# Optimization experiments

Measured on AMD Instinct MI355X. Metric: run time of the kernel, lower is better.

## Reference

```python
import jax, jax.numpy as jnp
import numpy as np
import math

L, D, H, V, B, S, MR = 8, 768, 12, 32000, 2, 1024, 4
HD = D // H

def setup_inputs() -> dict:
    key = jax.random.key(0)
    ks = iter(jax.random.split(key, 64))
    def rn(shape, s=0.02):
        return jax.random.normal(next(ks), shape, jnp.float32) * s
    inp = {}
    inp['tokens'] = jax.random.randint(next(ks), (B, S), 0, V, jnp.int32)
    inp['tok_emb'] = rn((V, D))
    inp['pos_emb'] = rn((S, D))
    for n in ['Wq_row', 'Wk_row', 'Wv_row', 'Wq_col', 'Wo']:
        inp[n] = rn((L, D, D))
    for n in ['bq_row', 'bk_row', 'bv_row', 'bq_col', 'bo']:
        inp[n] = jnp.zeros((L, D), jnp.float32)
    inp['ln1_g'] = jnp.ones((L, D), jnp.float32); inp['ln1_b'] = jnp.zeros((L, D), jnp.float32)
    inp['ln2_g'] = jnp.ones((L, D), jnp.float32); inp['ln2_b'] = jnp.zeros((L, D), jnp.float32)
    inp['W1'] = rn((L, D, MR * D)); inp['b1'] = jnp.zeros((L, MR * D), jnp.float32)
    inp['W2'] = rn((L, MR * D, D)); inp['b2'] = jnp.zeros((L, D), jnp.float32)
    inp['Wk_sh'] = rn((D, D)); inp['bk_sh'] = jnp.zeros((D,), jnp.float32)
    inp['Wv_sh'] = rn((D, D)); inp['bv_sh'] = jnp.zeros((D,), jnp.float32)
    inp['lnf_g'] = jnp.ones((D,), jnp.float32); inp['lnf_b'] = jnp.zeros((D,), jnp.float32)
    inp['Whead'] = rn((D, V)); inp['bhead'] = jnp.zeros((V,), jnp.float32)
    return inp

def _ln(x, g, b, eps=1e-5):
    m = x.mean(-1, keepdims=True)
    v = ((x - m) ** 2).mean(-1, keepdims=True)
    return (x - m) * jax.lax.rsqrt(v + eps) * g + b

def _heads(x):
    b, s, _ = x.shape
    return x.reshape(b, s, H, HD).transpose(0, 2, 1, 3)  # [B,H,S,hd]

def _merge(x):
    b, h, s, hd = x.shape
    return x.transpose(0, 2, 1, 3).reshape(b, s, h * hd)

def _forward(tokens, tok_emb, pos_emb, Wq_row, bq_row, Wk_row, bk_row, Wv_row, bv_row,
             Wq_col, bq_col, Wo, bo, ln1_g, ln1_b, ln2_g, ln2_b, W1, b1, W2, b2,
             Wk_sh, bk_sh, Wv_sh, bv_sh, lnf_g, lnf_b, Whead, bhead):
    s_len = tokens.shape[1]
    inv = 1.0 / math.sqrt(HD)
    x = tok_emb[tokens] + pos_emb[:s_len]
    mask = jnp.triu(jnp.ones((s_len, s_len), bool), 1)
    past_k, past_v = [], []
    for i in range(L):
        h = _ln(x, ln1_g[i], ln1_b[i])
        q_row = _heads(h @ Wq_row[i] + bq_row[i])
        k_row = _heads(h @ Wk_row[i] + bk_row[i])
        v_row = _heads(h @ Wv_row[i] + bv_row[i])
        q_col = _heads(h @ Wq_col[i] + bq_col[i])
        k_col = _heads(h @ Wk_sh + bk_sh)   # shared KV projector (archived memory)
        v_col = _heads(h @ Wv_sh + bv_sh)
        ts = jnp.einsum('bhqd,bhkd->bhqk', q_row, k_row) * inv
        ts = jnp.where(mask, -jnp.inf, ts)
        if past_k:
            pk = jnp.stack(past_k, axis=3)  # [B,H,S,l,hd]
            pv = jnp.stack(past_v, axis=3)
            ms = jnp.einsum('bhsd,bhsld->bhsl', q_col, pk) * inv
            w = jax.nn.softmax(jnp.concatenate([ts, ms], axis=-1), axis=-1)
            tw, mw = w[..., :s_len], w[..., s_len:]
            ctx = (jnp.einsum('bhqk,bhkd->bhqd', tw, v_row)
                   + jnp.einsum('bhsl,bhsld->bhsd', mw, pv))
        else:
            ctx = jnp.einsum('bhqk,bhkd->bhqd', jax.nn.softmax(ts, axis=-1), v_row)
        x = x + (_merge(ctx) @ Wo[i] + bo[i])
        h2 = _ln(x, ln2_g[i], ln2_b[i])
        x = x + (jax.nn.gelu(h2 @ W1[i] + b1[i], approximate=False) @ W2[i] + b2[i])
        past_k.append(k_col)
        past_v.append(v_col)
    return _ln(x, lnf_g, lnf_b) @ Whead + bhead

def reference(tokens, tok_emb, pos_emb, Wq_row, bq_row, Wk_row, bk_row, Wv_row, bv_row,
              Wq_col, bq_col, Wo, bo, ln1_g, ln1_b, ln2_g, ln2_b, W1, b1, W2, b2,
              Wk_sh, bk_sh, Wv_sh, bv_sh, lnf_g, lnf_b, Whead, bhead):
    return _forward(tokens, tok_emb, pos_emb, Wq_row, bq_row, Wk_row, bk_row, Wv_row, bv_row,
                    Wq_col, bq_col, Wo, bo, ln1_g, ln1_b, ln2_g, ln2_b, W1, b1, W2, b2,
                    Wk_sh, bk_sh, Wv_sh, bv_sh, lnf_g, lnf_b, Whead, bhead)
```

## Files before the change

### kernel.cpp

```cpp
#include <hip/hip_runtime.h>
#include <hip/hip_bf16.h>
#include <math.h>

#define L_   8
#define D_   768
#define H_   12
#define V_   32000
#define B_   2
#define S_   1024
#define HD_  64
#define BS_  2048
#define DFF_ 3072

typedef __hip_bfloat16 bf16;
typedef __attribute__((ext_vector_type(8))) short bf16x8;
typedef __attribute__((ext_vector_type(4))) float f32x4;

#define CFUN(r) (((r) >> 1) & 3)

__device__ __forceinline__ void cp16(void* lds, const void* g) {
  __builtin_amdgcn_global_load_lds(
      (const __attribute__((address_space(1))) void*)g,
      (__attribute__((address_space(3))) void*)lds, 16, 0, 0);
}

__device__ __forceinline__ unsigned short f2bf(float v) {
  __hip_bfloat16 h = __float2bfloat16(v);
  return *reinterpret_cast<unsigned short*>(&h);
}
__device__ __forceinline__ float bf2f(unsigned short u) {
  return __uint_as_float(((unsigned)u) << 16);
}

__global__ __launch_bounds__(256) void k_embed(const int* __restrict__ tokens,
    const float* __restrict__ tok_emb, const float* __restrict__ pos_emb,
    float* __restrict__ x) {
  int idx = blockIdx.x * 256 + threadIdx.x;
  int row = idx / D_;
  int d   = idx - row * D_;
  int s   = row & (S_ - 1);
  int t   = tokens[row];
  x[idx] = tok_emb[(size_t)t * D_ + d] + pos_emb[(size_t)s * D_ + d];
}

__global__ __launch_bounds__(256) void k_ln(const float* __restrict__ x,
    const float* __restrict__ g, const float* __restrict__ b,
    bf16* __restrict__ out) {
  int row = blockIdx.x;
  const float* xr = x + (size_t)row * D_;
  int t = threadIdx.x;
  float v0 = xr[t], v1 = xr[t + 256], v2 = xr[t + 512];
  float s  = v0 + v1 + v2;
  float s2 = v0 * v0 + v1 * v1 + v2 * v2;
#pragma unroll
  for (int off = 32; off; off >>= 1) {
    s  += __shfl_down(s, off);
    s2 += __shfl_down(s2, off);
  }
  __shared__ float rs[4], rs2[4];
  __shared__ float mean_s, rstd_s;
  int wid = t >> 6;
  if ((t & 63) == 0) { rs[wid] = s; rs2[wid] = s2; }
  __syncthreads();
  if (t == 0) {
    float S1 = rs[0] + rs[1] + rs[2] + rs[3];
    float S2 = rs2[0] + rs2[1] + rs2[2] + rs2[3];
    float m  = S1 / D_;
    float var = S2 / D_ - m * m;
    mean_s = m;
    rstd_s = rsqrtf(var + 1e-5f);
  }
  __syncthreads();
  float m = mean_s, r = rstd_s;
  bf16* orow = out + (size_t)row * D_;
  orow[t]       = __float2bfloat16((v0 - m) * r * g[t]       + b[t]);
  orow[t + 256] = __float2bfloat16((v1 - m) * r * g[t + 256] + b[t + 256]);
  orow[t + 512] = __float2bfloat16((v2 - m) * r * g[t + 512] + b[t + 512]);
}

__global__ __launch_bounds__(256) void k_redln(float* __restrict__ x,
    const float* __restrict__ pk, const float* __restrict__ b2,
    const float* __restrict__ g, const float* __restrict__ b,
    bf16* __restrict__ out) {
  const int row = blockIdx.x;
  const int t = threadIdx.x;
  const size_t base = (size_t)row * D_;
  const size_t MN = (size_t)BS_ * D_;
  float v0, v1, v2;
  {
    int c0 = t, c1 = t + 256, c2 = t + 512;
    v0 = x[base + c0] + pk[base + c0] + pk[MN + base + c0] + b2[c0];
    v1 = x[base + c1] + pk[base + c1] + pk[MN + base + c1] + b2[c1];
    v2 = x[base + c2] + pk[base + c2] + pk[MN + base + c2] + b2[c2];
    x[base + c0] = v0; x[base + c1] = v1; x[base + c2] = v2;
  }
  float s  = v0 + v1 + v2;
  float s2 = v0 * v0 + v1 * v1 + v2 * v2;
#pragma unroll
  for (int off = 32; off; off >>= 1) {
    s  += __shfl_down(s, off);
    s2 += __shfl_down(s2, off);
  }
  __shared__ float rs[4], rs2[4];
  __shared__ float mean_s, rstd_s;
  int wid = t >> 6;
  if ((t & 63) == 0) { rs[wid] = s; rs2[wid] = s2; }
  __syncthreads();
  if (t == 0) {
    float S1 = rs[0] + rs[1] + rs[2] + rs[3];
    float S2 = rs2[0] + rs2[1] + rs2[2] + rs2[3];
    float m  = S1 / D_;
    float var = S2 / D_ - m * m;
    mean_s = m;
    rstd_s = rsqrtf(var + 1e-5f);
  }
  __syncthreads();
  float m = mean_s, r = rstd_s;
  bf16* orow = out + base;
  orow[t]       = __float2bfloat16((v0 - m) * r * g[t]       + b[t]);
  orow[t + 256] = __float2bfloat16((v1 - m) * r * g[t + 256] + b[t + 256]);
  orow[t + 512] = __float2bfloat16((v2 - m) * r * g[t + 512] + b[t + 512]);
}

__global__ __launch_bounds__(256) void k_w2bf_t(const float* __restrict__ W,
    bf16* __restrict__ Wt, int K, int N, size_t ils, size_t ols) {
  __shared__ float t[32][33];
  const float* Wm = W + (size_t)blockIdx.z * ils;
  bf16* Wtm = Wt + (size_t)blockIdx.z * ols;
  int n0 = blockIdx.x * 32, k0 = blockIdx.y * 32;
  int tx = threadIdx.x;
  for (int i = threadIdx.y; i < 32; i += 8)
    t[i][tx] = Wm[(size_t)(k0 + i) * N + n0 + tx];
  __syncthreads();
  for (int i = threadIdx.y; i < 32; i += 8)
    Wtm[(size_t)(n0 + i) * K + k0 + tx] = __float2bfloat16(t[tx][i]);
}

__global__ __launch_bounds__(256) void k_bcat(const float* __restrict__ bq,
    const float* __restrict__ bk, const float* __restrict__ bqc,
    const float* __restrict__ bv, const float* __restrict__ bksh,
    const float* __restrict__ bvsh, float* __restrict__ b6) {
  int idx = blockIdx.x * 256 + threadIdx.x;
  if (idx >= L_ * 4608) return;
  int l = idx / 4608, c = idx - l * 4608;
  float v = (c < 768)  ? bq[l * 768 + c]
          : (c < 1536) ? bk[l * 768 + c - 768]
          : (c < 2304) ? bqc[l * 768 + c - 1536]
          : (c < 3072) ? bv[l * 768 + c - 2304]
          : (c < 3840) ? bksh[c - 3072]
                       : bvsh[c - 3840];
  b6[idx] = v;
}

template <int BM, int EPI, int KSPL>
__global__ __launch_bounds__(256) void k_bgemm(
    const bf16* __restrict__ A, const bf16* __restrict__ Wt,
    const bf16* __restrict__ Wt2,
    const float* __restrict__ bias, const float* __restrict__ resid,
    float* __restrict__ Cf, bf16* __restrict__ Cb, bf16* __restrict__ Cb2,
    bf16* __restrict__ Cb3, int NM, int M, int N, int K) {
  constexpr int ASZ = BM * 64;
  constexpr int ALINES = BM / 64;
  constexpr int BSTRIDE = ASZ + 8192;
  constexpr int MF = BM / 32;
  __shared__ __align__(16) char smem[3 * BSTRIDE];
  const int tid = threadIdx.x;
  const int l = tid & 63, w = tid >> 6;
  const int wr = w >> 1, wc = w & 1;

  const int nwg = (int)gridDim.x;
  int id = (int)blockIdx.x;
  id = (id & 7) * (nwg >> 3) + (id >> 3);
  int sk = 0;
  if constexpr (KSPL == 2) {
    const int TT = nwg >> 1;
    sk = id / TT;
    id -= sk * TT;
  }
  const int m0 = (id % NM) * BM;
  const int n0 = (id / NM) * 128;
  const int kstart = sk * (K / KSPL);

  const int lane15 = l & 15, lg = l >> 4;

  const bf16* WB = Wt;
  int nb0 = n0;
  if constexpr (EPI == 6) {
    if (n0 >= 3072) { WB = Wt2; nb0 = n0 - 3072; }
  }

  const int r0 = tid >> 2, p0 = tid & 3;
  const char* aSrc[ALINES];
#pragma unroll
  for (int i = 0; i < ALINES; i++) {
    const int rr = i * 64 + r0;
    aSrc[i] = (const char*)(A + (size_t)(m0 + rr) * K + kstart) + ((p0 ^ CFUN(rr)) * 16);
  }
  const char* bSrc0 = (const char*)(WB + (size_t)(nb0 + r0) * K + kstart) + ((p0 ^ CFUN(r0)) * 16);
  const char* bSrc1 = (const char*)(WB + (size_t)(nb0 + 64 + r0) * K + kstart) + ((p0 ^ CFUN(64 + r0)) * 16);

  int aOff[MF], bOff[4];
#pragma unroll
  for (int mi = 0; mi < MF; mi++) {
    int r = wr * (BM / 2) + mi * 16 + lane15;
    aOff[mi] = r * 64 + ((lg ^ CFUN(r)) * 16);
  }
#pragma unroll
  for (int ni = 0; ni < 4; ni++) {
    int r = wc * 64 + ni * 16 + lane15;
    bOff[ni] = ASZ + r * 64 + ((lg ^ CFUN(r)) * 16);
  }

  f32x4 acc[MF][4];
#pragma unroll
  for (int mi = 0; mi < MF; mi++)
#pragma unroll
    for (int ni = 0; ni < 4; ni++) acc[mi][ni] = (f32x4){0.f, 0.f, 0.f, 0.f};

  auto stage = [&](int buf, int t) {
    const size_t kb = (size_t)t * 64;
    char* base = smem + buf * BSTRIDE;
#pragma unroll
    for (int i = 0; i < ALINES; i++)
      cp16(base + i * 4096 + w * 1024, aSrc[i] + kb);
    cp16(base + ASZ + w * 1024, bSrc0 + kb);
    cp16(base + ASZ + 4096 + w * 1024, bSrc1 + kb);
  };
  auto compute = [&](int buf) {
    const char* base = smem + buf * BSTRIDE;
    bf16x8 af[MF], bfr[4];
#pragma unroll
    for (int mi = 0; mi < MF; mi++) af[mi] = *(const bf16x8*)(base + aOff[mi]);
#pragma unroll
    for (int ni = 0; ni < 4; ni++) bfr[ni] = *(const bf16x8*)(base + bOff[ni]);
    __builtin_amdgcn_s_setprio(1);
#pragma unroll
    for (int mi = 0; mi < MF; mi++)
#pragma unroll
      for (int ni = 0; ni < 4; ni++)
        acc[mi][ni] = __builtin_amdgcn_mfma_f32_16x16x32_bf16(
            af[mi], bfr[ni], acc[mi][ni], 0, 0, 0);
    __builtin_amdgcn_s_setprio(0);
  };

  const int nk = (K / KSPL) >> 5;
  stage(0, 0);
  stage(1, 1);
  int buf = 0;
  for (int t = 0; t < nk; t++) {
    if (t + 1 < nk) {
      if constexpr (ALINES == 2) asm volatile("s_waitcnt vmcnt(4)" ::: "memory");
      else                       asm volatile("s_waitcnt vmcnt(3)" ::: "memory");
    } else {
      asm volatile("s_waitcnt vmcnt(0)" ::: "memory");
    }
    __builtin_amdgcn_s_barrier();
    if (t + 2 < nk) {
      int nb = buf + 2; if (nb >= 3) nb -= 3;
      stage(nb, t + 2);
    }
    compute(buf);
    buf = (buf == 2) ? 0 : buf + 1;
  }

#pragma unroll
  for (int ni = 0; ni < 4; ni++) {
    const int col = n0 + wc * 64 + ni * 16 + lane15;
    const float bv = bias[col];
#pragma unroll
    for (int mi = 0; mi < MF; mi++) {
      const int rowb = m0 + wr * (BM / 2) + mi * 16 + lg * 4;
      if constexpr (EPI == 6) {
        if (col < 2304) {
#pragma unroll
          for (int j = 0; j < 4; j++)
            Cb[(size_t)(rowb + j) * 2304 + col] = __float2bfloat16(acc[mi][ni][j] + bv);
        } else if (col < 3072) {
          ushort4 pk;
          pk.x = f2bf(acc[mi][ni][0] + bv);
          pk.y = f2bf(acc[mi][ni][1] + bv);
          pk.z = f2bf(acc[mi][ni][2] + bv);
          pk.w = f2bf(acc[mi][ni][3] + bv);
          const int bq = rowb >> 10, s = rowb & (S_ - 1);
          *reinterpret_cast<ushort4*>(
              (unsigned short*)Cb2 + ((size_t)(bq * 768 + (col - 2304))) * S_ + s) = pk;
        } else {
#pragma unroll
          for (int j = 0; j < 4; j++)
            Cb3[(size_t)(rowb + j) * 1536 + (col - 3072)] =
                __float2bfloat16(acc[mi][ni][j] + bv);
        }
      } else if constexpr (EPI == 7) {
#pragma unroll
        for (int j = 0; j < 4; j++)
          Cf[(size_t)sk * M * N + (size_t)(rowb + j) * N + col] = acc[mi][ni][j];
      } else {
#pragma unroll
        for (int j = 0; j < 4; j++) {
          const int row = rowb + j;
          float v = acc[mi][ni][j] + bv;
          if constexpr (EPI == 1) v += resid[(size_t)row * N + col];
          if constexpr (EPI == 2) {
            v = 0.5f * v * (1.0f + erff(v * 0.70710678118654752f));
            Cb[(size_t)row * N + col] = __float2bfloat16(v);
          } else if constexpr (EPI == 3) {
            Cb[(size_t)row * N + col] = __float2bfloat16(v);
          } else {
            Cf[(size_t)row * N + col] = v;
          }
        }
      }
    }
  }
}

#define HBAR() asm volatile("s_barrier" ::: "memory")
#define MFMA16(AF, BF, MB, NB)                                               \
  do {                                                                       \
    __builtin_amdgcn_s_setprio(1);                                           \
    _Pragma("unroll") for (int mi_ = 0; mi_ < 4; mi_++)                      \
      _Pragma("unroll") for (int ni_ = 0; ni_ < 2; ni_++)                    \
        _Pragma("unroll") for (int ks_ = 0; ks_ < 2; ks_++)                  \
          acc[(MB) + mi_][(NB) + ni_] =                                      \
              __builtin_amdgcn_mfma_f32_16x16x32_bf16(                       \
                  AF[mi_][ks_], BF[ni_][ks_], acc[(MB) + mi_][(NB) + ni_],   \
                  0, 0, 0);                                                  \
    __builtin_amdgcn_s_setprio(0);                                           \
  } while (0)

__global__ __launch_bounds__(512, 1) void k_head8(const bf16* __restrict__ A,
    const bf16* __restrict__ Wt, const float* __restrict__ bias,
    float* __restrict__ C) {
  __shared__ __align__(16) char smem[131072];
  const int tid = threadIdx.x;
  const int l = tid & 63, w = tid >> 6;
  const int wr = w >> 2, wc = w & 3;
  const int lane15 = l & 15, lg = l >> 4;

  int id = (int)blockIdx.x;
  id = (id & 7) * 125 + (id >> 3);
  const int m0 = (id % 8) * 256;
  const int n0 = (id / 8) * 256;

  auto issueA = [&](int tile, int hb) {
#pragma unroll
    for (int j = 0; j < 2; j++) {
      const int idx = j * 512 + tid;
      const int rl = idx >> 3, sl = idx & 7;
      const bf16* g = A + (size_t)(m0 + hb + rl) * 768 + tile * 64 +
                      ((sl ^ (rl & 7)) << 3);
      cp16(smem + (tile & 1) * 32768 + hb * 128 + (j * 512 + w * 64) * 16, g);
    }
  };
  auto issueB = [&](int tile, int hb) {
#pragma unroll
    for (int j = 0; j < 2; j++) {
      const int idx = j * 512 + tid;
      const int rl = idx >> 3, sl = idx & 7;
      const bf16* g = Wt + (size_t)(n0 + hb + rl) * 768 + tile * 64 +
                      ((sl ^ (rl & 7)) << 3);
      cp16(smem + 65536 + (tile & 1) * 32768 + hb * 128 + (j * 512 + w * 64) * 16, g);
    }
  };
  auto ldA = [&](int buf, int mi, int ks) {
    const int r = wr * 128 + mi * 16 + lane15;
    return *(const bf16x8*)(smem + buf * 32768 + r * 128 +
                            ((((ks << 2) + lg) ^ (r & 7)) << 4));
  };
  auto ldB = [&](int buf, int ni, int ks) {
    const int r = wc * 64 + ni * 16 + lane15;
    return *(const bf16x8*)(smem + 65536 + buf * 32768 + r * 128 +
                            ((((ks << 2) + lg) ^ (r & 7)) << 4));
  };

  f32x4 acc[8][4];
#pragma unroll
  for (int i = 0; i < 8; i++)
#pragma unroll
    for (int j = 0; j < 4; j++) acc[i][j] = (f32x4){0.f, 0.f, 0.f, 0.f};
  bf16x8 alo[4][2], ahi[4][2], blo[2][2], bhi[2][2];

  issueA(0, 0);  issueA(0, 128);  issueB(0, 0);  issueB(0, 128);
  issueB(1, 0);  issueA(1, 0);    issueB(1, 128);
  asm volatile("s_waitcnt vmcnt(6)" ::: "memory");
  HBAR();

  for (int it = 0; it < 5; ++it) {
    const int Tb = 2 * it + 1, Tn = 2 * it + 2;
#pragma unroll
    for (int mi = 0; mi < 4; mi++) { alo[mi][0] = ldA(0, mi, 0); alo[mi][1] = ldA(0, mi, 1); }
#pragma unroll
    for (int ni = 0; ni < 2; ni++) { blo[ni][0] = ldB(0, ni, 0); blo[ni][1] = ldB(0, ni, 1); }
    issueA(Tb, 128);
    HBAR(); MFMA16(alo, blo, 0, 0); HBAR();
#pragma unroll
    for (int ni = 0; ni < 2; ni++) { bhi[ni][0] = ldB(0, ni + 2, 0); bhi[ni][1] = ldB(0, ni + 2, 1); }
    HBAR(); MFMA16(alo, bhi, 0, 2); HBAR();
#pragma unroll
    for (int mi = 0; mi < 4; mi++) { ahi[mi][0] = ldA(0, mi + 4, 0); ahi[mi][1] = ldA(0, mi + 4, 1); }
    issueB(Tn, 0);
    HBAR(); MFMA16(ahi, bhi, 4, 2); HBAR();
    issueA(Tn, 0);
    issueB(Tn, 128);
    asm volatile("s_waitcnt vmcnt(6)" ::: "memory");
    HBAR(); MFMA16(ahi, blo, 4, 0); HBAR();
#pragma unroll
    for (int mi = 0; mi < 4; mi++) { alo[mi][0] = ldA(1, mi, 0); alo[mi][1] = ldA(1, mi, 1); }
#pragma unroll
    for (int ni = 0; ni < 2; ni++) { blo[ni][0] = ldB(1, ni, 0); blo[ni][1] = ldB(1, ni, 1); }
    issueA(Tn, 128);
    HBAR(); MFMA16(alo, blo, 0, 0); HBAR();
#pragma unroll
    for (int ni = 0; ni < 2; ni++) { bhi[ni][0] = ldB(1, ni + 2, 0); bhi[ni][1] = ldB(1, ni + 2, 1); }
    HBAR(); MFMA16(alo, bhi, 0, 2); HBAR();
#pragma unroll
    for (int mi = 0; mi < 4; mi++) { ahi[mi][0] = ldA(1, mi + 4, 0); ahi[mi][1] = ldA(1, mi + 4, 1); }
    issueB(Tn + 1, 0);
    HBAR(); MFMA16(ahi, bhi, 4, 2); HBAR();
    issueA(Tn + 1, 0);
    issueB(Tn + 1, 128);
    asm volatile("s_waitcnt vmcnt(6)" ::: "memory");
    HBAR(); MFMA16(ahi, blo, 4, 0); HBAR();
  }

  {
#pragma unroll
    for (int mi = 0; mi < 4; mi++) { alo[mi][0] = ldA(0, mi, 0); alo[mi][1] = ldA(0, mi, 1); }
#pragma unroll
    for (int ni = 0; ni < 2; ni++) { blo[ni][0] = ldB(0, ni, 0); blo[ni][1] = ldB(0, ni, 1); }
    issueA(11, 128);
    HBAR(); MFMA16(alo, blo, 0, 0); HBAR();
#pragma unroll
    for (int ni = 0; ni < 2; ni++) { bhi[ni][0] = ldB(0, ni + 2, 0); bhi[ni][1] = ldB(0, ni + 2, 1); }
    HBAR(); MFMA16(alo, bhi, 0, 2); HBAR();
#pragma unroll
    for (int mi = 0; mi < 4; mi++) { ahi[mi][0] = ldA(0, mi + 4, 0); ahi[mi][1] = ldA(0, mi + 4, 1); }
    HBAR(); MFMA16(ahi, bhi, 4, 2); HBAR();
    asm volatile("s_waitcnt vmcnt(0)" ::: "memory");
    HBAR(); MFMA16(ahi, blo, 4, 0); HBAR();
#pragma unroll
    for (int mi = 0; mi < 4; mi++) { alo[mi][0] = ldA(1, mi, 0); alo[mi][1] = ldA(1, mi, 1); }
#pragma unroll
    for (int ni = 0; ni < 2; ni++) { blo[ni][0] = ldB(1, ni, 0); blo[ni][1] = ldB(1, ni, 1); }
    MFMA16(alo, blo, 0, 0);
#pragma unroll
    for (int ni = 0; ni < 2; ni++) { bhi[ni][0] = ldB(1, ni + 2, 0); bhi[ni][1] = ldB(1, ni + 2, 1); }
    MFMA16(alo, bhi, 0, 2);
#pragma unroll
    for (int mi = 0; mi < 4; mi++) { ahi[mi][0] = ldA(1, mi + 4, 0); ahi[mi][1] = ldA(1, mi + 4, 1); }
    MFMA16(ahi, bhi, 4, 2);
    MFMA16(ahi, blo, 4, 0);
  }

#pragma unroll
  for (int ni = 0; ni < 4; ni++) {
    const int col = n0 + wc * 64 + ni * 16 + lane15;
    const float bv = bias[col];
#pragma unroll
    for (int mi = 0; mi < 8; mi++) {
      const int rowb = m0 + wr * 128 + mi * 16 + lg * 4;
#pragma unroll
      for (int j = 0; j < 4; j++)
        C[(size_t)(rowb + j) * 32000 + col] = acc[mi][ni][j] + bv;
    }
  }
}

__global__ __launch_bounds__(256) void k_attn(
    const bf16* __restrict__ qkv, const bf16* __restrict__ vT,
    const bf16* __restrict__ memkv, bf16* __restrict__ ctx, int layer) {
  const int bh = blockIdx.x;
  const int b = bh / H_, h = bh % H_;
  const int qt = (int)gridDim.y - 1 - (int)blockIdx.y;
  const int tid = threadIdx.x;
  const int w = tid >> 6, l = tid & 63;
  const int lane15 = l & 15, lg = l >> 4;
  const float inv = 0.125f;

  __shared__ char plds[4][2048];
  __shared__ float wlp[4][16][16];
  char* pl = plds[w];

  const int qrow0 = qt * 64 + w * 16;
  const size_t rowA = (size_t)(b * S_ + qrow0 + lane15);
  const bf16* qp = qkv + rowA * 2304 + h * 64 + lg * 8;
  auto scale8 = [](bf16x8 v) {
    bf16x8 r;
#pragma unroll
    for (int e = 0; e < 8; e++)
      r[e] = (short)f2bf(bf2f((unsigned short)v[e]) * 0.125f);
    return r;
  };
  const bf16x8 qf0 = scale8(*(const bf16x8*)(qp));
  const bf16x8 qf1 = scale8(*(const bf16x8*)(qp + 32));

  const bf16* kbase = qkv + (size_t)(b * S_) * 2304 + 768 + h * 64 + lg * 8;
  const bf16* vbase = vT + ((size_t)(b * 768 + h * 64 + lane15)) * S_;

  float mrow[4], dsum[4];
  f32x4 acc[4];
#pragma unroll
  for (int j = 0; j < 4; j++) { mrow[j] = -INFINITY; dsum[j] = 0.f; }
#pragma unroll
  for (int ni = 0; ni < 4; ni++) acc[ni] = (f32x4){0.f, 0.f, 0.f, 0.f};

  const int ntile = ((qrow0 + 15) >> 6) + 1;
  for (int kt64 = 0; kt64 < ntile; kt64++) {
    const int k0 = kt64 * 64;
    f32x4 sc[4];
#pragma unroll
    for (int kt = 0; kt < 4; kt++) {
      const bf16* kp = kbase + (size_t)(k0 + kt * 16 + lane15) * 2304;
      bf16x8 kf0 = *(const bf16x8*)(kp);
      bf16x8 kf1 = *(const bf16x8*)(kp + 32);
      f32x4 z = (f32x4){0.f, 0.f, 0.f, 0.f};
      z = __builtin_amdgcn_mfma_f32_16x16x32_bf16(qf0, kf0, z, 0, 0, 0);
      sc[kt] = __builtin_amdgcn_mfma_f32_16x16x32_bf16(qf1, kf1, z, 0, 0, 0);
    }
    float tmax[4];
#pragma unroll
    for (int j = 0; j < 4; j++) tmax[j] = -INFINITY;
    const bool needMask = (k0 + 63 > qrow0);
    if (needMask) {
#pragma unroll
      for (int kt = 0; kt < 4; kt++) {
        const int kabs = k0 + kt * 16 + lane15;
#pragma unroll
        for (int j = 0; j < 4; j++) {
          const int qabs = qrow0 + lg * 4 + j;
          float v = (kabs <= qabs) ? sc[kt][j] : -INFINITY;
          sc[kt][j] = v;
          tmax[j] = fmaxf(tmax[j], v);
        }
      }
    } else {
#pragma unroll
      for (int kt = 0; kt < 4; kt++)
#pragma unroll
        for (int j = 0; j < 4; j++) tmax[j] = fmaxf(tmax[j], sc[kt][j]);
    }
#pragma unroll
    for (int off = 1; off < 16; off <<= 1)
#pragma unroll
      for (int j = 0; j < 4; j++) tmax[j] = fmaxf(tmax[j], __shfl_xor(tmax[j], off, 16));

    bool grow = false;
#pragma unroll
    for (int j = 0; j < 4; j++) grow |= (tmax[j] > mrow[j]);
    if (__ballot(grow) != 0ull) {
#pragma unroll
      for (int j = 0; j < 4; j++) {
        const float mnew = fmaxf(mrow[j], tmax[j]);
        const float alpha = __expf(mrow[j] - mnew);
        mrow[j] = mnew;
        dsum[j] *= alpha;
#pragma unroll
        for (int ni = 0; ni < 4; ni++) acc[ni][j] *= alpha;
      }
    }
    float psum[4] = {0.f, 0.f, 0.f, 0.f};
#pragma unroll
    for (int kt = 0; kt < 4; kt++) {
      const int gsl = kt * 2 + (lane15 >> 3);
      const int ebyte = (lane15 & 7) * 2;
#pragma unroll
      for (int j = 0; j < 4; j++) {
        const float p = __expf(sc[kt][j] - mrow[j]);
        psum[j] += p;
        const int r = lg * 4 + j;
        *(unsigned short*)(pl + r * 128 + ((gsl ^ (r & 7)) << 4) + ebyte) = f2bf(p);
      }
    }
#pragma unroll
    for (int off = 1; off < 16; off <<= 1)
#pragma unroll
      for (int j = 0; j < 4; j++) psum[j] += __shfl_xor(psum[j], off, 16);
#pragma unroll
    for (int j = 0; j < 4; j++) dsum[j] += psum[j];

#pragma unroll
    for (int ks = 0; ks < 2; ks++) {
      bf16x8 pa = *(const bf16x8*)(pl + lane15 * 128 +
                                   ((((ks << 2) + lg) ^ (lane15 & 7)) << 4));
      const bf16* vp = vbase + k0 + ks * 32 + lg * 8;
#pragma unroll
      for (int ni = 0; ni < 4; ni++) {
        bf16x8 vf = *(const bf16x8*)(vp + (size_t)ni * 16 * S_);
        acc[ni] = __builtin_amdgcn_mfma_f32_16x16x32_bf16(pa, vf, acc[ni], 0, 0, 0);
      }
    }
  }

  const int r4 = lg * 4;
  if (lane15 < layer) {
    const int ml = lane15;
#pragma unroll
    for (int j = 0; j < 4; j++) {
      const size_t rowB = (size_t)(b * S_) + qrow0 + r4 + j;
      const bf16* qc = qkv + rowB * 2304 + 1536 + h * 64;
      const bf16* mk = memkv + ((size_t)ml * BS_ + rowB) * 1536 + h * 64;
      float d_ = 0.f;
#pragma unroll
      for (int t = 0; t < 8; t++) {
        bf16x8 qv = *(const bf16x8*)(qc + t * 8);
        bf16x8 kv = *(const bf16x8*)(mk + t * 8);
#pragma unroll
        for (int e = 0; e < 8; e++)
          d_ += bf2f((unsigned short)qv[e]) * bf2f((unsigned short)kv[e]);
      }
      wlp[w][r4 + j][ml] = d_ * inv;
    }
  }
  if (layer > 0) {
#pragma unroll
    for (int j = 0; j < 4; j++) {
      const int r = r4 + j;
      float mm = -INFINITY;
      for (int ml = 0; ml < layer; ml++) mm = fmaxf(mm, wlp[w][r][ml]);
      const float mnew = fmaxf(mrow[j], mm);
      const float alpha = __expf(mrow[j] - mnew);
      mrow[j] = mnew;
      dsum[j] *= alpha;
#pragma unroll
      for (int ni = 0; ni < 4; ni++) acc[ni][j] *= alpha;
      const size_t rowB = (size_t)(b * S_) + qrow0 + r;
      for (int ml = 0; ml < layer; ml++) {
        const float p = __expf(wlp[w][r][ml] - mnew);
        dsum[j] += p;
        const unsigned short* mv = (const unsigned short*)(memkv +
            ((size_t)ml * BS_ + rowB) * 1536 + 768 + h * 64 + lane15);
#pragma unroll
        for (int ni = 0; ni < 4; ni++)
          acc[ni][j] += p * bf2f(mv[ni * 16]);
      }
    }
  }

#pragma unroll
  for (int j = 0; j < 4; j++) {
    const float rd = 1.f / dsum[j];
    const size_t rowB = (size_t)(b * S_) + qrow0 + r4 + j;
    bf16* cp = ctx + rowB * 768 + h * 64 + lane15;
#pragma unroll
    for (int ni = 0; ni < 4; ni++)
      cp[ni * 16] = __float2bfloat16(acc[ni][j] * rd);
  }
}

extern "C" void kernel_launch(void* const* d_in, const int* in_sizes, int n_in,
                              void* d_out, int out_size, void* d_ws, size_t ws_size,
                              hipStream_t stream) {
  const int*   tokens  = (const int*)d_in[0];
  const float* tok_emb = (const float*)d_in[1];
  const float* pos_emb = (const float*)d_in[2];
  const float *Wq_row, *Wk_row, *Wv_row, *Wq_col, *Wo;
  const float *bq_row, *bk_row, *bv_row, *bq_col, *bo;
  if (in_sizes[4] == L_ * D_ * D_) {
    Wq_row = (const float*)d_in[3];  Wk_row = (const float*)d_in[4];
    Wv_row = (const float*)d_in[5];  Wq_col = (const float*)d_in[6];
    Wo     = (const float*)d_in[7];
    bq_row = (const float*)d_in[8];  bk_row = (const float*)d_in[9];
    bv_row = (const float*)d_in[10]; bq_col = (const float*)d_in[11];
    bo     = (const float*)d_in[12];
  } else {
    Wq_row = (const float*)d_in[3];  bq_row = (const float*)d_in[4];
    Wk_row = (const float*)d_in[5];  bk_row = (const float*)d_in[6];
    Wv_row = (const float*)d_in[7];  bv_row = (const float*)d_in[8];
    Wq_col = (const float*)d_in[9];  bq_col = (const float*)d_in[10];
    Wo     = (const float*)d_in[11]; bo     = (const float*)d_in[12];
  }
  const float* ln1_g = (const float*)d_in[13]; const float* ln1_b = (const float*)d_in[14];
  const float* ln2_g = (const float*)d_in[15]; const float* ln2_b = (const float*)d_in[16];
  const float* W1    = (const float*)d_in[17]; const float* b1    = (const float*)d_in[18];
  const float* W2    = (const float*)d_in[19]; const float* b2    = (const float*)d_in[20];
  const float* Wk_sh = (const float*)d_in[21]; const float* bk_sh = (const float*)d_in[22];
  const float* Wv_sh = (const float*)d_in[23]; const float* bv_sh = (const float*)d_in[24];
  const float* lnf_g = (const float*)d_in[25]; const float* lnf_b = (const float*)d_in[26];
  const float* Whead = (const float*)d_in[27]; const float* bhead = (const float*)d_in[28];

  char* p = (char*)d_ws;
  float* x      = (float*)p; p += (size_t)BS_ * D_ * 4;
  bf16*  h_bf   = (bf16*)p;  p += (size_t)BS_ * D_ * 2;
  bf16*  qkv3   = (bf16*)p;  p += (size_t)BS_ * 2304 * 2;
  bf16*  vTb    = (bf16*)p;  p += (size_t)B_ * 768 * S_ * 2;
  bf16*  memkv  = (bf16*)p;  p += (size_t)L_ * BS_ * 1536 * 2;
  bf16*  ctx_bf = (bf16*)p;  p += (size_t)BS_ * D_ * 2;
  bf16*  mlp_bf = (bf16*)p;  p += (size_t)BS_ * DFF_ * 2;
  float* pkbuf  = (float*)p; p += (size_t)2 * BS_ * D_ * 4;
  float* b6cat  = (float*)p; p += (size_t)L_ * 4608 * 4;
  bf16* tW6    = (bf16*)p; p += (size_t)L_ * 3072 * D_ * 2;
  bf16* tWsh   = (bf16*)p; p += (size_t)1536 * D_ * 2;
  bf16* tWo    = (bf16*)p; p += (size_t)L_ * D_ * D_ * 2;
  bf16* tW1    = (bf16*)p; p += (size_t)L_ * DFF_ * D_ * 2;
  bf16* tW2    = (bf16*)p; p += (size_t)L_ * D_ * DFF_ * 2;
  bf16* tWhead = (bf16*)p; p += (size_t)V_ * D_ * 2;

  dim3 tb(32, 8);
  const size_t DD = (size_t)D_ * D_;
  const size_t W6S = (size_t)3072 * 768;
  k_w2bf_t<<<dim3(24, 24, L_), tb, 0, stream>>>(Wq_row, tW6,              768, 768, DD, W6S);
  k_w2bf_t<<<dim3(24, 24, L_), tb, 0, stream>>>(Wk_row, tW6 + 768 * 768,  768, 768, DD, W6S);
  k_w2bf_t<<<dim3(24, 24, L_), tb, 0, stream>>>(Wq_col, tW6 + 1536 * 768, 768, 768, DD, W6S);
  k_w2bf_t<<<dim3(24, 24, L_), tb, 0, stream>>>(Wv_row, tW6 + 2304 * 768, 768, 768, DD, W6S);
  k_w2bf_t<<<dim3(24, 24, 1), tb, 0, stream>>>(Wk_sh, tWsh,             768, 768, 0, 0);
  k_w2bf_t<<<dim3(24, 24, 1), tb, 0, stream>>>(Wv_sh, tWsh + 768 * 768, 768, 768, 0, 0);
  k_w2bf_t<<<dim3(24, 24, L_), tb, 0, stream>>>(Wo,     tWo, 768, 768, DD, DD);
  k_w2bf_t<<<dim3(96, 24, L_), tb, 0, stream>>>(W1, tW1, 768, 3072, (size_t)768 * 3072, (size_t)3072 * 768);
  k_w2bf_t<<<dim3(24, 96, L_), tb, 0, stream>>>(W2, tW2, 3072, 768, (size_t)768 * 3072, (size_t)768 * 3072);
  k_w2bf_t<<<dim3(1000, 24, 1), tb, 0, stream>>>(Whead, tWhead, 768, 32000, 0, 0);
  k_bcat<<<dim3(144), 256, 0, stream>>>(bq_row, bk_row, bq_col, bv_row, bk_sh, bv_sh, b6cat);

  k_embed<<<dim3((BS_ * D_) / 256), 256, 0, stream>>>(tokens, tok_emb, pos_emb, x);
  k_ln<<<dim3(BS_), 256, 0, stream>>>(x, ln1_g, ln1_b, h_bf);

  for (int i = 0; i < L_; i++) {
    k_bgemm<128, 6, 1><<<dim3(576), 256, 0, stream>>>(
        h_bf, tW6 + (size_t)i * W6S, tWsh, b6cat + (size_t)i * 4608,
        nullptr, nullptr, qkv3, vTb, memkv + (size_t)i * BS_ * 1536,
        16, BS_, 4608, 768);
    k_attn<<<dim3(B_ * H_, S_ / 64), 256, 0, stream>>>(qkv3, vTb, memkv, ctx_bf, i);
    k_bgemm<64, 7, 2><<<dim3(384), 256, 0, stream>>>(
        ctx_bf, tWo + (size_t)i * DD, nullptr, bo + i * D_,
        nullptr, pkbuf, nullptr, nullptr, nullptr, 32, BS_, 768, 768);
    k_redln<<<dim3(BS_), 256, 0, stream>>>(x, pkbuf, bo + i * D_,
                                           ln2_g + i * D_, ln2_b + i * D_, h_bf);
    k_bgemm<128, 2, 1><<<dim3(384), 256, 0, stream>>>(
        h_bf, tW1 + (size_t)i * 3072 * 768, nullptr, b1 + (size_t)i * DFF_,
        nullptr, nullptr, mlp_bf, nullptr, nullptr, 16, BS_, 3072, 768);
    k_bgemm<64, 7, 2><<<dim3(384), 256, 0, stream>>>(
        mlp_bf, tW2 + (size_t)i * 768 * 3072, nullptr, b2 + i * D_,
        nullptr, pkbuf, nullptr, nullptr, nullptr, 32, BS_, 768, 3072);
    const float* gn = (i < L_ - 1) ? (ln1_g + (i + 1) * D_) : lnf_g;
    const float* bn = (i < L_ - 1) ? (ln1_b + (i + 1) * D_) : lnf_b;
    k_redln<<<dim3(BS_), 256, 0, stream>>>(x, pkbuf, b2 + i * D_, gn, bn, h_bf);
  }
  k_head8<<<dim3(1000), 512, 0, stream>>>(h_bf, tWhead, bhead, (float*)d_out);
}
```

Measured before the change: 1.637 ms.

## Route fused QKV projection through 256x256 head GEMM kernel and vectorize weight transpose stores

The fused QKV/shared-KV projection (N=4608) now runs on the large 256x256-tile, 512-thread GEMM kernel previously used only for the LM head. That kernel is templated over an epilogue so it can write the split bf16 outputs, including the transposed V. The aim is more data reuse per tile and fewer blocks, at the cost of 144 blocks that may underfill the GPU's compute units. The weight transpose kernel also now writes four bf16 values per store instead of scalar stores.

```diff
diff --git a/kernel.cpp b/kernel.cpp
--- a/kernel.cpp
+++ b/kernel.cpp
@@ -128,12 +128,19 @@
   const float* Wm = W + (size_t)blockIdx.z * ils;
   bf16* Wtm = Wt + (size_t)blockIdx.z * ols;
   int n0 = blockIdx.x * 32, k0 = blockIdx.y * 32;
-  int tx = threadIdx.x;
-  for (int i = threadIdx.y; i < 32; i += 8)
+  int tx = threadIdx.x, ty = threadIdx.y;
+  for (int i = ty; i < 32; i += 8)
     t[i][tx] = Wm[(size_t)(k0 + i) * N + n0 + tx];
   __syncthreads();
-  for (int i = threadIdx.y; i < 32; i += 8)
-    Wtm[(size_t)(n0 + i) * K + k0 + tx] = __float2bfloat16(t[tx][i]);
+  const int tlin = ty * 32 + tx;
+  const int n = tlin >> 3;
+  const int kq = (tlin & 7) * 4;
+  ushort4 o;
+  o.x = f2bf(t[kq + 0][n]);
+  o.y = f2bf(t[kq + 1][n]);
+  o.z = f2bf(t[kq + 2][n]);
+  o.w = f2bf(t[kq + 3][n]);
+  *reinterpret_cast<ushort4*>((unsigned short*)Wtm + (size_t)(n0 + n) * K + k0 + kq) = o;
 }
 
 __global__ __launch_bounds__(256) void k_bcat(const float* __restrict__ bq,
@@ -155,10 +162,9 @@
 template <int BM, int EPI, int KSPL>
 __global__ __launch_bounds__(256) void k_bgemm(
     const bf16* __restrict__ A, const bf16* __restrict__ Wt,
-    const bf16* __restrict__ Wt2,
     const float* __restrict__ bias, const float* __restrict__ resid,
-    float* __restrict__ Cf, bf16* __restrict__ Cb, bf16* __restrict__ Cb2,
-    bf16* __restrict__ Cb3, int NM, int M, int N, int K) {
+    float* __restrict__ Cf, bf16* __restrict__ Cb,
+    int NM, int M, int N, int K) {
   constexpr int ASZ = BM * 64;
   constexpr int ALINES = BM / 64;
   constexpr int BSTRIDE = ASZ + 8192;
@@ -183,12 +189,6 @@
 
   const int lane15 = l & 15, lg = l >> 4;
 
-  const bf16* WB = Wt;
-  int nb0 = n0;
-  if constexpr (EPI == 6) {
-    if (n0 >= 3072) { WB = Wt2; nb0 = n0 - 3072; }
-  }
-
   const int r0 = tid >> 2, p0 = tid & 3;
   const char* aSrc[ALINES];
 #pragma unroll
@@ -196,8 +196,8 @@
     const int rr = i * 64 + r0;
     aSrc[i] = (const char*)(A + (size_t)(m0 + rr) * K + kstart) + ((p0 ^ CFUN(rr)) * 16);
   }
-  const char* bSrc0 = (const char*)(WB + (size_t)(nb0 + r0) * K + kstart) + ((p0 ^ CFUN(r0)) * 16);
-  const char* bSrc1 = (const char*)(WB + (size_t)(nb0 + 64 + r0) * K + kstart) + ((p0 ^ CFUN(64 + r0)) * 16);
+  const char* bSrc0 = (const char*)(Wt + (size_t)(n0 + r0) * K + kstart) + ((p0 ^ CFUN(r0)) * 16);
+  const char* bSrc1 = (const char*)(Wt + (size_t)(n0 + 64 + r0) * K + kstart) + ((p0 ^ CFUN(64 + r0)) * 16);
 
   int aOff[MF], bOff[4];
 #pragma unroll
@@ -270,27 +270,7 @@
 #pragma unroll
     for (int mi = 0; mi < MF; mi++) {
       const int rowb = m0 + wr * (BM / 2) + mi * 16 + lg * 4;
-      if constexpr (EPI == 6) {
-        if (col < 2304) {
-#pragma unroll
-          for (int j = 0; j < 4; j++)
-            Cb[(size_t)(rowb + j) * 2304 + col] = __float2bfloat16(acc[mi][ni][j] + bv);
-        } else if (col < 3072) {
-          ushort4 pk;
-          pk.x = f2bf(acc[mi][ni][0] + bv);
-          pk.y = f2bf(acc[mi][ni][1] + bv);
-          pk.z = f2bf(acc[mi][ni][2] + bv);
-          pk.w = f2bf(acc[mi][ni][3] + bv);
-          const int bq = rowb >> 10, s = rowb & (S_ - 1);
-          *reinterpret_cast<ushort4*>(
-              (unsigned short*)Cb2 + ((size_t)(bq * 768 + (col - 2304))) * S_ + s) = pk;
-        } else {
-#pragma unroll
-          for (int j = 0; j < 4; j++)
-            Cb3[(size_t)(rowb + j) * 1536 + (col - 3072)] =
-                __float2bfloat16(acc[mi][ni][j] + bv);
-        }
-      } else if constexpr (EPI == 7) {
+      if constexpr (EPI == 7) {
 #pragma unroll
         for (int j = 0; j < 4; j++)
           Cf[(size_t)sk * M * N + (size_t)(rowb + j) * N + col] = acc[mi][ni][j];
@@ -328,19 +308,28 @@
     __builtin_amdgcn_s_setprio(0);                                           \
   } while (0)
 
-__global__ __launch_bounds__(512, 1) void k_head8(const bf16* __restrict__ A,
-    const bf16* __restrict__ Wt, const float* __restrict__ bias,
-    float* __restrict__ C) {
+template <int EPI>
+__global__ __launch_bounds__(512, 1) void k_g8(const bf16* __restrict__ A,
+    const bf16* __restrict__ Wt, const bf16* __restrict__ Wt2,
+    const float* __restrict__ bias, float* __restrict__ Cf,
+    bf16* __restrict__ Cb, bf16* __restrict__ Cb2, bf16* __restrict__ Cb3) {
   __shared__ __align__(16) char smem[131072];
   const int tid = threadIdx.x;
   const int l = tid & 63, w = tid >> 6;
   const int wr = w >> 2, wc = w & 3;
   const int lane15 = l & 15, lg = l >> 4;
 
+  const int nwg = (int)gridDim.x;
   int id = (int)blockIdx.x;
-  id = (id & 7) * 125 + (id >> 3);
+  id = (id & 7) * (nwg >> 3) + (id >> 3);
   const int m0 = (id % 8) * 256;
   const int n0 = (id / 8) * 256;
+
+  const bf16* WB = Wt;
+  int nb0 = n0;
+  if constexpr (EPI == 6) {
+    if (n0 >= 3072) { WB = Wt2; nb0 = n0 - 3072; }
+  }
 
   auto issueA = [&](int tile, int hb) {
 #pragma unroll
@@ -357,7 +346,7 @@
     for (int j = 0; j < 2; j++) {
       const int idx = j * 512 + tid;
       const int rl = idx >> 3, sl = idx & 7;
-      const bf16* g = Wt + (size_t)(n0 + hb + rl) * 768 + tile * 64 +
+      const bf16* g = WB + (size_t)(nb0 + hb + rl) * 768 + tile * 64 +
                       ((sl ^ (rl & 7)) << 3);
       cp16(smem + 65536 + (tile & 1) * 32768 + hb * 128 + (j * 512 + w * 64) * 16, g);
     }
@@ -459,9 +448,31 @@
 #pragma unroll
     for (int mi = 0; mi < 8; mi++) {
       const int rowb = m0 + wr * 128 + mi * 16 + lg * 4;
-#pragma unroll
-      for (int j = 0; j < 4; j++)
-        C[(size_t)(rowb + j) * 32000 + col] = acc[mi][ni][j] + bv;
+      if constexpr (EPI == 0) {
+#pragma unroll
+        for (int j = 0; j < 4; j++)
+          Cf[(size_t)(rowb + j) * 32000 + col] = acc[mi][ni][j] + bv;
+      } else {
+        if (col < 2304) {
+#pragma unroll
+          for (int j = 0; j < 4; j++)
+            Cb[(size_t)(rowb + j) * 2304 + col] = __float2bfloat16(acc[mi][ni][j] + bv);
+        } else if (col < 3072) {
+          ushort4 pk;
+          pk.x = f2bf(acc[mi][ni][0] + bv);
+          pk.y = f2bf(acc[mi][ni][1] + bv);
+          pk.z = f2bf(acc[mi][ni][2] + bv);
+          pk.w = f2bf(acc[mi][ni][3] + bv);
+          const int bq = rowb >> 10, s = rowb & (S_ - 1);
+          *reinterpret_cast<ushort4*>(
+              (unsigned short*)Cb2 + ((size_t)(bq * 768 + (col - 2304))) * S_ + s) = pk;
+        } else {
+#pragma unroll
+          for (int j = 0; j < 4; j++)
+            Cb3[(size_t)(rowb + j) * 1536 + (col - 3072)] =
+                __float2bfloat16(acc[mi][ni][j] + bv);
+        }
+      }
     }
   }
 }
@@ -714,25 +725,25 @@
   k_ln<<<dim3(BS_), 256, 0, stream>>>(x, ln1_g, ln1_b, h_bf);
 
   for (int i = 0; i < L_; i++) {
-    k_bgemm<128, 6, 1><<<dim3(576), 256, 0, stream>>>(
+    k_g8<6><<<dim3(144), 512, 0, stream>>>(
         h_bf, tW6 + (size_t)i * W6S, tWsh, b6cat + (size_t)i * 4608,
-        nullptr, nullptr, qkv3, vTb, memkv + (size_t)i * BS_ * 1536,
-        16, BS_, 4608, 768);
+        nullptr, qkv3, vTb, memkv + (size_t)i * BS_ * 1536);
     k_attn<<<dim3(B_ * H_, S_ / 64), 256, 0, stream>>>(qkv3, vTb, memkv, ctx_bf, i);
     k_bgemm<64, 7, 2><<<dim3(384), 256, 0, stream>>>(
-        ctx_bf, tWo + (size_t)i * DD, nullptr, bo + i * D_,
-        nullptr, pkbuf, nullptr, nullptr, nullptr, 32, BS_, 768, 768);
+        ctx_bf, tWo + (size_t)i * DD, bo + i * D_,
+        nullptr, pkbuf, nullptr, 32, BS_, 768, 768);
     k_redln<<<dim3(BS_), 256, 0, stream>>>(x, pkbuf, bo + i * D_,
                                            ln2_g + i * D_, ln2_b + i * D_, h_bf);
     k_bgemm<128, 2, 1><<<dim3(384), 256, 0, stream>>>(
-        h_bf, tW1 + (size_t)i * 3072 * 768, nullptr, b1 + (size_t)i * DFF_,
-        nullptr, nullptr, mlp_bf, nullptr, nullptr, 16, BS_, 3072, 768);
+        h_bf, tW1 + (size_t)i * 3072 * 768, b1 + (size_t)i * DFF_,
+        nullptr, nullptr, mlp_bf, 16, BS_, 3072, 768);
     k_bgemm<64, 7, 2><<<dim3(384), 256, 0, stream>>>(
-        mlp_bf, tW2 + (size_t)i * 768 * 3072, nullptr, b2 + i * D_,
-        nullptr, pkbuf, nullptr, nullptr, nullptr, 32, BS_, 768, 3072);
+        mlp_bf, tW2 + (size_t)i * 768 * 3072, b2 + i * D_,
+        nullptr, pkbuf, nullptr, 32, BS_, 768, 3072);
     const float* gn = (i < L_ - 1) ? (ln1_g + (i + 1) * D_) : lnf_g;
     const float* bn = (i < L_ - 1) ? (ln1_b + (i + 1) * D_) : lnf_b;
     k_redln<<<dim3(BS_), 256, 0, stream>>>(x, pkbuf, b2 + i * D_, gn, bn, h_bf);
   }
-  k_head8<<<dim3(1000), 512, 0, stream>>>(h_bf, tWhead, bhead, (float*)d_out);
-}
+  k_g8<0><<<dim3(1000), 512, 0, stream>>>(h_bf, tWhead, nullptr, bhead,
+                                          (float*)d_out, nullptr, nullptr, nullptr);
+}
```

New measurement: 1.630 ms. Within noise of the previous version (-0.4%).
